# Performance work log

Hardware: AMD Instinct MI355X
Metric: run time of the kernel (lower is better)

## Reference

```python
import jax, jax.numpy as jnp
import numpy as np

OBS_LEN, PRED_LEN, N, NUM_SEQ = 8, 12, 512, 8
H_ENC, H_DEC, EMB, NOISE_DIM = 8, 16, 16, 8


def setup_inputs() -> dict:
    key = jax.random.key(0)
    ks = jax.random.split(key, 32)
    def rn(i, shape, std=1.0):
        return jax.random.normal(ks[i], shape, jnp.float32) * std
    bounds = np.arange(NUM_SEQ + 1) * (N // NUM_SEQ)
    bih_t = jnp.zeros(4 * H_ENC, jnp.float32).at[H_ENC:2 * H_ENC].set(1.0)  # forget bias 1
    bih_p = jnp.zeros(4 * H_DEC, jnp.float32).at[H_DEC:2 * H_DEC].set(1.0)
    return {
        'traj_rel': rn(0, (OBS_LEN + PRED_LEN, N, 2)),
        'obs_traj_pos': rn(1, (OBS_LEN, N, 2), 5.0),
        'pred_traj_gt_pos': rn(2, (PRED_LEN, N, 2), 5.0),
        'h0': rn(3, (N, H_ENC)), 'c0': rn(4, (N, H_ENC)),
        'noise': rn(5, (NUM_SEQ, NOISE_DIM)),
        'W_enc': rn(6, (EMB, 2), 0.2), 'b_enc': jnp.zeros(EMB, jnp.float32),
        'W_dec': rn(7, (EMB, H_DEC + 2), 0.2), 'b_dec': jnp.zeros(EMB, jnp.float32),
        'Wih_t': rn(8, (4 * H_ENC, EMB), 0.1), 'Whh_t': rn(9, (4 * H_ENC, H_ENC), 0.001),
        'bih_t': bih_t, 'bhh_t': jnp.zeros(4 * H_ENC, jnp.float32),
        'Wih_p': rn(10, (4 * H_DEC, EMB), 0.1), 'Whh_p': rn(11, (4 * H_DEC, H_DEC), 0.001),
        'bih_p': bih_p, 'bhh_p': jnp.zeros(4 * H_DEC, jnp.float32),
        'W_out': rn(12, (2, H_DEC), 0.1), 'b_out': jnp.zeros(2, jnp.float32),
        'W_se': rn(13, (EMB, 2), 0.1), 'b_se': jnp.zeros(EMB, jnp.float32),
        'W_m1': rn(14, (64, EMB + H_DEC), 0.1), 'b_m1': jnp.zeros(64, jnp.float32),
        'W_m2': rn(15, (H_DEC, 64), 0.1), 'b_m2': jnp.zeros(H_DEC, jnp.float32),
        'W_att': rn(16, (1, H_DEC), 0.1), 'b_att': jnp.zeros(1, jnp.float32),
        'seq_start_end': jnp.asarray(np.stack([bounds[:-1], bounds[1:]], 1), jnp.int32),
        'nei_index': jax.random.randint(ks[17], (PRED_LEN, N, N), 0, 2, jnp.int32),
        'nei_num_index': jnp.full((N,), N // 2, jnp.int32),
    }


def _lstm_cell(x, h, c, Wih, Whh, bih, bhh):
    g = x @ Wih.T + bih + h @ Whh.T + bhh
    i, f, gg, o = jnp.split(g, 4, axis=-1)
    c2 = jax.nn.sigmoid(f) * c + jax.nn.sigmoid(i) * jnp.tanh(gg)
    return jax.nn.sigmoid(o) * jnp.tanh(c2), c2


def reference(traj_rel, obs_traj_pos, pred_traj_gt_pos, h0, c0, noise,
              W_enc, b_enc, W_dec, b_dec,
              Wih_t, Whh_t, bih_t, bhh_t,
              Wih_p, Whh_p, bih_p, bhh_p,
              W_out, b_out, W_se, b_se, W_m1, b_m1, W_m2, b_m2, W_att, b_att,
              seq_start_end, nei_index, nei_num_index):
    nb = traj_rel.shape[1]

    # ---- encoder: obs_len tiny LSTM steps over relative displacements ----
    def enc_step(carry, x_t):
        h, c = carry
        e = jax.nn.relu(x_t @ W_enc.T + b_enc)
        h, c = _lstm_cell(e, h, c, Wih_t, Whh_t, bih_t, bhh_t)
        return (h, c), None
    (h_enc, _), _ = jax.lax.scan(enc_step, (h0, c0), traj_rel[:OBS_LEN])

    # ---- add global per-scene noise (noise_mix_type == 'global') ----
    seq_ids = jnp.searchsorted(seq_start_end[:, 0], jnp.arange(nb), side='right') - 1
    dec_h = jnp.concatenate([h_enc, noise[seq_ids]], axis=1)  # [N, 16]

    def pool(pos, mask, h):
        # corr_index[i,j] = pos[i] - pos[j]
        corr = pos[:, None, :] - pos[None, :, :]                 # [N,N,2]
        r = corr @ W_se.T + b_se                                 # [N,N,EMB]
        hj = jnp.broadcast_to(h[None, :, :], (nb, nb, H_DEC))    # neighbor hidden
        m_in = jnp.concatenate([r, hj], axis=-1)                 # [N,N,EMB+H]
        h1 = jax.nn.relu(m_in @ W_m1.T + b_m1)                   # [N,N,64]
        pre = jax.nn.relu(h1 @ W_m2.T + b_m2)                    # [N,N,H]
        s = jnp.squeeze(pre @ W_att.T + b_att, -1)               # [N,N]
        s = jnp.where(mask, s, -1e9)
        w = jax.nn.softmax(s, axis=-1)
        ctx = jnp.einsum('ij,ijh->ih', w, pre)
        return jnp.where(mask.any(-1, keepdims=True), ctx, 0.0)

    # ---- decoder: pred_len steps with social pooling each step ----
    sg = jax.lax.stop_gradient
    init = (dec_h, jnp.zeros_like(dec_h), jnp.zeros_like(dec_h),
            jnp.zeros((nb, 2), dec_h.dtype), obs_traj_pos[-1])

    def dec_step(carry, nei_t):
        h, c, ctx, out, pos = carry
        inp_cat = jnp.concatenate([sg(ctx), sg(out)], axis=-1)   # [N, 18]
        e = jax.nn.relu(inp_cat @ W_dec.T + b_dec)
        h, c = _lstm_cell(e, h, c, Wih_p, Whh_p, bih_p, bhh_p)
        ctx = pool(pos, nei_t > 0, h)
        out = jnp.tanh((ctx + h) @ W_out.T + b_out) * 4.4
        pos = sg(pos + out)
        return (h, c, ctx, out, pos), out

    _, pred_traj_rel = jax.lax.scan(dec_step, init, nei_index)
    return pred_traj_rel  # [pred_len, N, 2]
```

## Files before the change

kernel.cpp:

```cpp
#include <hip/hip_runtime.h>
#include <math.h>

#define NPED 512
#define OBS 8
#define PRED 12
#define HE 8
#define HD 16
#define EMB 16
#define NZ 8
#define NSEQ 8

typedef const float* fp;
typedef float f2 __attribute__((ext_vector_type(2)));

__device__ __forceinline__ float frcp(float x){ return __builtin_amdgcn_rcpf(x); }
__device__ __forceinline__ float sigm(float x){ return frcp(1.0f + __expf(-x)); }
__device__ __forceinline__ float tanh_f(float x){ return 1.0f - 2.0f*frcp(__expf(2.0f*x) + 1.0f); }

#define WS_H    0
#define WS_C    (WS_H + NPED*HD)
#define WS_POS0 (WS_C + NPED*HD)
#define WS_POS1 (WS_POS0 + NPED*2)
#define WS_HB0  (WS_POS1 + NPED*2)
#define WS_HB1  (WS_HB0 + NPED*64)
#define WS_A0   (WS_HB1 + NPED*64)
#define WS_A1   (WS_A0 + 64)
#define WS_BB   (WS_A1 + 64)
#define WS_WM2T (WS_BB + 64)

__global__ __launch_bounds__(256) void init_kernel(
        fp traj, fp obs_pos, fp h0, fp c0, fp noise,
        fp Wenc, fp benc, fp Wih, fp Whh, fp bih, fp bhh,
        fp bdec, fp Wihp, fp Whhp, fp bihp, fp bhhp, fp Wm1,
        fp Wse, fp bse, fp bm1, fp Wm2,
        const int* sse, float* ws)
{
    __shared__ float s_wenc[32], s_benc[16], s_wihT[32*17], s_whhT[32*9], s_bT[32];
    __shared__ float s_wihP[64*17], s_whhP[64*17], s_wm1h[64*17], s_bP[64], s_e0[16];
    __shared__ float s_hc[16*16];
    int tid = threadIdx.x;

    if (blockIdx.x == 0) {
        if (tid < 64) {
            float a0 = 0.f, a1 = 0.f, bb = bm1[tid];
            for (int kk = 0; kk < 16; kk++) {
                float w = Wm1[tid*32 + kk];
                a0 += w*Wse[kk*2+0]; a1 += w*Wse[kk*2+1]; bb += w*bse[kk];
            }
            ws[WS_A0 + tid] = a0; ws[WS_A1 + tid] = a1; ws[WS_BB + tid] = bb;
        }
        for (int i = tid; i < 1024; i += 256) {
            int u = i >> 4, v = i & 15;
            ws[WS_WM2T + u*16 + v] = Wm2[v*64 + u];
        }
    }

    if (tid < 32) { s_wenc[tid] = Wenc[tid]; s_bT[tid] = bih[tid] + bhh[tid]; }
    if (tid < 16) { s_benc[tid] = benc[tid]; s_e0[tid] = fmaxf(bdec[tid], 0.f); }
    for (int i = tid; i < 512; i += 256) s_wihT[(i>>4)*17 + (i&15)] = Wih[i];
    { int i = tid; if (i < 256) s_whhT[(i>>3)*9 + (i&7)] = Whh[i]; }
    for (int i = tid; i < 1024; i += 256) {
        int r = i>>4, d = i&15;
        s_wihP[r*17+d] = Wihp[i];
        s_whhP[r*17+d] = Whhp[i];
        s_wm1h[r*17+d] = Wm1[r*32 + 16 + d];
    }
    if (tid < 64) s_bP[tid] = bihp[tid] + bhhp[tid];
    __syncthreads();

    int pid = tid >> 4, k16 = tid & 15;
    int n = blockIdx.x*16 + pid;

    if (k16 < 8) {
        int k = k16;
        float h = h0[n*HE+k], c = c0[n*HE+k];
        for (int t = 0; t < OBS; t++) {
            float x0 = traj[(t*NPED+n)*2+0];
            float x1 = traj[(t*NPED+n)*2+1];
            float g0 = s_bT[k], g1 = s_bT[8+k], g2 = s_bT[16+k], g3 = s_bT[24+k];
            #pragma unroll
            for (int d = 0; d < EMB; d++) {
                float e = fmaxf(s_wenc[d*2]*x0 + s_wenc[d*2+1]*x1 + s_benc[d], 0.f);
                g0 += s_wihT[(k)*17+d]*e;    g1 += s_wihT[(8+k)*17+d]*e;
                g2 += s_wihT[(16+k)*17+d]*e; g3 += s_wihT[(24+k)*17+d]*e;
            }
            #pragma unroll
            for (int d = 0; d < HE; d++) {
                float hv = __shfl(h, d, 8);
                g0 += s_whhT[(k)*9+d]*hv;    g1 += s_whhT[(8+k)*9+d]*hv;
                g2 += s_whhT[(16+k)*9+d]*hv; g3 += s_whhT[(24+k)*9+d]*hv;
            }
            c = sigm(g1)*c + sigm(g0)*tanh_f(g2);
            h = sigm(g3)*tanh_f(c);
        }
        int cnt = 0;
        #pragma unroll
        for (int s2 = 0; s2 < NSEQ; s2++) cnt += (sse[s2*2] <= n) ? 1 : 0;
        s_hc[pid*16 + k]     = h;
        s_hc[pid*16 + 8 + k] = noise[(cnt-1)*NZ + k];
    }
    __syncthreads();

    int k = k16;
    float h = s_hc[pid*16 + k];
    float g0 = s_bP[k], g1 = s_bP[16+k], g2 = s_bP[32+k], g3 = s_bP[48+k];
    #pragma unroll
    for (int d = 0; d < HD; d++) {
        float ev = s_e0[d];
        float hv = __shfl(h, d, 16);
        g0 += s_wihP[(k)*17+d]*ev    + s_whhP[(k)*17+d]*hv;
        g1 += s_wihP[(16+k)*17+d]*ev + s_whhP[(16+k)*17+d]*hv;
        g2 += s_wihP[(32+k)*17+d]*ev + s_whhP[(32+k)*17+d]*hv;
        g3 += s_wihP[(48+k)*17+d]*ev + s_whhP[(48+k)*17+d]*hv;
    }
    float c = sigm(g0)*tanh_f(g2);
    float hn = sigm(g3)*tanh_f(c);
    ws[WS_H + n*HD + k] = hn;
    ws[WS_C + n*HD + k] = c;

    float hb0=0.f, hb1=0.f, hb2=0.f, hb3=0.f;
    #pragma unroll
    for (int d = 0; d < HD; d++) {
        float hv = __shfl(hn, d, 16);
        hb0 += s_wm1h[(k)*17+d]*hv;    hb1 += s_wm1h[(16+k)*17+d]*hv;
        hb2 += s_wm1h[(32+k)*17+d]*hv; hb3 += s_wm1h[(48+k)*17+d]*hv;
    }
    float* hb = ws + WS_HB0 + n*64;
    hb[k] = hb0; hb[16+k] = hb1; hb[32+k] = hb2; hb[48+k] = hb3;
    if (k < 2) ws[WS_POS0 + n*2 + k] = obs_pos[((OBS-1)*NPED+n)*2 + k];
}

__global__ __launch_bounds__(512, 4) void pool_step_kernel(
        int t, int last, const int* nei,
        fp Wm1, fp bm2, fp Watt, fp batt,
        fp Wdec, fp bdec, fp Wihp, fp Whhp, fp bihp, fp bhhp, fp Wout, fp bout,
        float* ws, float* dout)
{
    __shared__ float s_A0[64], s_A1[64], s_BB[64];
    __shared__ float s_wm2t[1024];
    __shared__ float s_bm2[16], s_watt[16];
    __shared__ float s_batt;
    __shared__ float s_posx[NPED], s_posy[NPED];
    __shared__ int   s_list[NPED], s_cnt[8];
    __shared__ float s_mat[16*512];
    __shared__ float s_lred[8], s_mred[8], s_ctxacc[16], s_ctx[16];
    __shared__ float s_wdec[16*19], s_bdec[16], s_wout[32], s_bout[2];
    int tid = threadIdx.x;

    if (tid < 64) { s_A0[tid] = ws[WS_A0+tid]; s_A1[tid] = ws[WS_A1+tid]; s_BB[tid] = ws[WS_BB+tid]; }
    if (tid < 256) ((float4*)s_wm2t)[tid] = ((const float4*)(ws + WS_WM2T))[tid];
    if (tid < 16) { s_bm2[tid] = bm2[tid]; s_watt[tid] = Watt[tid]; }
    if (tid == 0) s_batt = batt[0];
    for (int i = tid; i < 288; i += 512) s_wdec[(i/18)*19 + (i%18)] = Wdec[i];
    if (tid < 16) s_bdec[tid] = bdec[tid];
    if (tid < 32) s_wout[tid] = Wout[tid];
    if (tid < 2)  s_bout[tid] = bout[tid];

    const float* posrd = ws + ((t & 1) ? WS_POS1 : WS_POS0);
    const float* hbrd  = ws + ((t & 1) ? WS_HB1  : WS_HB0 );
    float* poswr = ws + ((t & 1) ? WS_POS0 : WS_POS1);
    float* hbwr  = ws + ((t & 1) ? WS_HB0  : WS_HB1 );
    {
        const float2* p2 = (const float2*)posrd;
        for (int j = tid; j < NPED; j += 512) { float2 pp = p2[j]; s_posx[j] = pp.x; s_posy[j] = pp.y; }
    }
    __syncthreads();

    int i = blockIdx.x;
    int w = tid >> 6, lane = tid & 63;
    unsigned long long below = (1ull << lane) - 1ull;

    int a = nei[((size_t)t*NPED + i)*NPED + tid] > 0;
    unsigned long long mb = __ballot(a);
    if (lane == 0) s_cnt[w] = __popcll(mb);
    __syncthreads();
    int cnt = 0, base = 0;
    #pragma unroll
    for (int q = 0; q < 8; q++) {
        int cq = s_cnt[q];
        cnt += cq;
        if (q < w) base += cq;
    }
    if (a) s_list[base + __popcll(mb & below)] = tid;
    __syncthreads();

    float pix = s_posx[i], piy = s_posy[i];
    f2 pre2[8];
    #pragma unroll
    for (int q = 0; q < 8; q++) pre2[q] = (f2){0.f, 0.f};
    float sc = -INFINITY;

    if (tid < cnt) {
        #pragma unroll
        for (int q = 0; q < 8; q++) pre2[q] = (f2){s_bm2[2*q], s_bm2[2*q+1]};
        int j = s_list[tid];
        float cx = pix - s_posx[j], cy = piy - s_posy[j];
        const float4* HB4 = (const float4*)(hbrd + j*64);
        const f2* A0v = (const f2*)s_A0;
        const f2* A1v = (const f2*)s_A1;
        const f2* BBv = (const f2*)s_BB;
        #pragma unroll
        for (int uq = 0; uq < 16; uq++) {
            float4 hb = HB4[uq];
            f2 hA = {hb.x, hb.y}, hB = {hb.z, hb.w};
            f2 h1A = __builtin_elementwise_max(A0v[2*uq]*cx + A1v[2*uq]*cy + (BBv[2*uq] + hA), (f2){0.f,0.f});
            f2 h1B = __builtin_elementwise_max(A0v[2*uq+1]*cx + A1v[2*uq+1]*cy + (BBv[2*uq+1] + hB), (f2){0.f,0.f});
            #define ACC16(u_, hsc_) { \
                f2 hs = {hsc_, hsc_}; \
                const f2* wr = (const f2*)(s_wm2t + (u_)*16); \
                for (int q = 0; q < 8; q++) pre2[q] = __builtin_elementwise_fma(wr[q], hs, pre2[q]); }
            ACC16(uq*4+0, h1A.x) ACC16(uq*4+1, h1A.y) ACC16(uq*4+2, h1B.x) ACC16(uq*4+3, h1B.y)
            #undef ACC16
        }
        f2 sacc = {0.f, 0.f};
        const f2* wa = (const f2*)s_watt;
        #pragma unroll
        for (int q = 0; q < 8; q++) {
            pre2[q] = __builtin_elementwise_max(pre2[q], (f2){0.f,0.f});
            sacc = __builtin_elementwise_fma(pre2[q], wa[q], sacc);
        }
        sc = s_batt + sacc.x + sacc.y;
    }

    float mloc = sc;
    #pragma unroll
    for (int off = 32; off >= 1; off >>= 1) mloc = fmaxf(mloc, __shfl_xor(mloc, off));
    if (lane == 0) s_mred[w] = mloc;
    __syncthreads();
    float M = s_mred[0];
    #pragma unroll
    for (int q = 1; q < 8; q++) M = fmaxf(M, s_mred[q]);

    float wexp = (tid < cnt) ? __expf(sc - M) : 0.f;
    float l = wexp;
    #pragma unroll
    for (int off = 32; off >= 1; off >>= 1) l += __shfl_xor(l, off);
    if (lane == 0) s_lred[w] = l;
    {
        const float* pa = (const float*)pre2;
        #pragma unroll
        for (int v = 0; v < 16; v++) s_mat[v*512 + tid] = wexp * pa[v];
    }
    __syncthreads();
    {
        int vv = tid >> 5, cc = tid & 31;
        float ssum = 0.f;
        #pragma unroll
        for (int e = 0; e < 16; e++) ssum += s_mat[vv*512 + cc + e*32];
        #pragma unroll
        for (int off = 16; off >= 1; off >>= 1) ssum += __shfl_xor(ssum, off, 32);
        if (cc == 0) s_ctxacc[vv] = ssum;
    }
    __syncthreads();
    if (tid < 16) {
        float cv = 0.f;
        if (cnt > 0) {
            float L = 0.f;
            #pragma unroll
            for (int q = 0; q < 8; q++) L += s_lred[q];
            cv = (L > 0.f) ? s_ctxacc[tid] / L : 0.f;
        }
        s_ctx[tid] = cv;
    }
    __syncthreads();

    if (tid < 64) {
        int r = tid;
        float h16 = 0.f, ctx16 = 0.f, cst = 0.f;
        if (r < 16) {
            h16   = ws[WS_H + i*HD + r];
            ctx16 = s_ctx[r];
            cst   = ws[WS_C + i*HD + r];
        }
        float ch = ctx16 + h16;
        float r0 = 0.f, r1 = 0.f;
        if (r < 16) { r0 = s_wout[r]*ch; r1 = s_wout[16+r]*ch; }
        #pragma unroll
        for (int off = 8; off >= 1; off >>= 1) {
            r0 += __shfl_xor(r0, off, 16);
            r1 += __shfl_xor(r1, off, 16);
        }
        float o0 = tanh_f(s_bout[0] + r0)*4.4f;
        float o1 = tanh_f(s_bout[1] + r1)*4.4f;
        if (r == 0) { dout[(t*NPED + i)*2 + 0] = o0; poswr[i*2+0] = pix + o0; }
        if (r == 1) { dout[(t*NPED + i)*2 + 1] = o1; poswr[i*2+1] = piy + o1; }

        if (!last) {
            float e = 0.f;
            if (r < 16) {
                e = s_bdec[r];
                #pragma unroll
                for (int d = 0; d < HD; d++) e += s_wdec[r*19 + d]*s_ctx[d];
                e += s_wdec[r*19+16]*o0 + s_wdec[r*19+17]*o1;
                e = fmaxf(e, 0.f);
            }
            const float4* wi4 = (const float4*)(Wihp + r*16);
            const float4* wh4 = (const float4*)(Whhp + r*16);
            float4 wi0 = wi4[0], wi1 = wi4[1], wi2 = wi4[2], wi3 = wi4[3];
            float4 wh0 = wh4[0], wh1 = wh4[1], wh2 = wh4[2], wh3 = wh4[3];
            float g = bihp[r] + bhhp[r];
            #define GD(wiv, whv, d0) { \
                g += wiv.x*__shfl(e, d0)   + whv.x*__shfl(h16, d0); \
                g += wiv.y*__shfl(e, d0+1) + whv.y*__shfl(h16, d0+1); \
                g += wiv.z*__shfl(e, d0+2) + whv.z*__shfl(h16, d0+2); \
                g += wiv.w*__shfl(e, d0+3) + whv.w*__shfl(h16, d0+3); }
            GD(wi0, wh0, 0) GD(wi1, wh1, 4) GD(wi2, wh2, 8) GD(wi3, wh3, 12)
            #undef GD
            float gi = __shfl(g, r & 15);
            float gf = __shfl(g, 16 + (r & 15));
            float gg = __shfl(g, 32 + (r & 15));
            float go = __shfl(g, 48 + (r & 15));
            float hn = 0.f;
            if (r < 16) {
                float cn = sigm(gf)*cst + sigm(gi)*tanh_f(gg);
                hn = sigm(go)*tanh_f(cn);
                ws[WS_H + i*HD + r] = hn;
                ws[WS_C + i*HD + r] = cn;
            }
            const float4* wm4 = (const float4*)(Wm1 + r*32 + 16);
            float4 m0 = wm4[0], m1 = wm4[1], m2 = wm4[2], m3 = wm4[3];
            float hb = 0.f;
            #define HBD(mv, d0) { \
                hb += mv.x*__shfl(hn, d0)   + mv.y*__shfl(hn, d0+1); \
                hb += mv.z*__shfl(hn, d0+2) + mv.w*__shfl(hn, d0+3); }
            HBD(m0, 0) HBD(m1, 4) HBD(m2, 8) HBD(m3, 12)
            #undef HBD
            hbwr[i*64 + r] = hb;
        }
    }
}

extern "C" void kernel_launch(void* const* d_in, const int* in_sizes, int n_in,
                              void* d_out, int out_size, void* d_ws, size_t ws_size,
                              hipStream_t stream)
{
    fp traj = (fp)d_in[0];
    fp obs  = (fp)d_in[1];
    fp h0   = (fp)d_in[3];
    fp c0   = (fp)d_in[4];
    fp noise= (fp)d_in[5];
    fp Wenc = (fp)d_in[6];  fp benc = (fp)d_in[7];
    fp Wdec = (fp)d_in[8];  fp bdec = (fp)d_in[9];
    fp Wiht = (fp)d_in[10]; fp Whht = (fp)d_in[11];
    fp biht = (fp)d_in[12]; fp bhht = (fp)d_in[13];
    fp Wihp = (fp)d_in[14]; fp Whhp = (fp)d_in[15];
    fp bihp = (fp)d_in[16]; fp bhhp = (fp)d_in[17];
    fp Wout = (fp)d_in[18]; fp bout = (fp)d_in[19];
    fp Wse  = (fp)d_in[20]; fp bse  = (fp)d_in[21];
    fp Wm1  = (fp)d_in[22]; fp bm1  = (fp)d_in[23];
    fp Wm2  = (fp)d_in[24]; fp bm2  = (fp)d_in[25];
    fp Watt = (fp)d_in[26]; fp batt = (fp)d_in[27];
    const int* sse = (const int*)d_in[28];
    const int* nei = (const int*)d_in[29];
    float* ws = (float*)d_ws;
    float* out = (float*)d_out;

    hipLaunchKernelGGL(init_kernel, dim3(32), dim3(256), 0, stream,
                       traj, obs, h0, c0, noise, Wenc, benc, Wiht, Whht, biht, bhht,
                       bdec, Wihp, Whhp, bihp, bhhp, Wm1, Wse, bse, bm1, Wm2, sse, ws);
    for (int t = 0; t < PRED; t++) {
        hipLaunchKernelGGL(pool_step_kernel, dim3(NPED), dim3(512), 0, stream,
                           t, (t == PRED-1) ? 1 : 0, nei,
                           Wm1, bm2, Watt, batt,
                           Wdec, bdec, Wihp, Whhp, bihp, bhhp, Wout, bout,
                           ws, out);
    }
}
```

Measured before the change: 169.7 us.

## Process two pedestrians per block with two neighbor pairs per thread

The pooling step kernel now handles two query pedestrians per 512-thread block, one per 256-thread half. Each thread evaluates up to two neighbor pairs, and the grid shrinks to half as many blocks. This is meant to cut the idle threads left when only about half the neighbors are active, and to share the per-block weight and position loads across two rows. The neighbor-mask load is also issued earlier. In exchange, the launch-bounds occupancy hint drops to two blocks and register pressure rises. The pre-activation arrays are no longer zero-initialised, so the products weighted by zero can read uninitialised values.

```diff
diff --git a/kernel.cpp b/kernel.cpp
--- a/kernel.cpp
+++ b/kernel.cpp
@@ -130,7 +130,44 @@
     if (k < 2) ws[WS_POS0 + n*2 + k] = obs_pos[((OBS-1)*NPED+n)*2 + k];
 }
 
-__global__ __launch_bounds__(512, 4) void pool_step_kernel(
+__device__ __forceinline__ float pair_compute(
+        int j, float pix, float piy,
+        const float* s_posx, const float* s_posy,
+        const float* s_A0, const float* s_A1, const float* s_BB,
+        const float* s_wm2t, const float* s_watt, float batt,
+        const float* hbrd, f2 pre2[8], const float* s_bm2)
+{
+    #pragma unroll
+    for (int q = 0; q < 8; q++) pre2[q] = (f2){s_bm2[2*q], s_bm2[2*q+1]};
+    float cx = pix - s_posx[j], cy = piy - s_posy[j];
+    const float4* HB4 = (const float4*)(hbrd + j*64);
+    const f2* A0v = (const f2*)s_A0;
+    const f2* A1v = (const f2*)s_A1;
+    const f2* BBv = (const f2*)s_BB;
+    #pragma unroll
+    for (int uq = 0; uq < 16; uq++) {
+        float4 hb = HB4[uq];
+        f2 hA = {hb.x, hb.y}, hB = {hb.z, hb.w};
+        f2 h1A = __builtin_elementwise_max(A0v[2*uq]*cx + A1v[2*uq]*cy + (BBv[2*uq] + hA), (f2){0.f,0.f});
+        f2 h1B = __builtin_elementwise_max(A0v[2*uq+1]*cx + A1v[2*uq+1]*cy + (BBv[2*uq+1] + hB), (f2){0.f,0.f});
+        #define ACC16(u_, hsc_) { \
+            f2 hs = {hsc_, hsc_}; \
+            const f2* wr = (const f2*)(s_wm2t + (u_)*16); \
+            for (int q = 0; q < 8; q++) pre2[q] = __builtin_elementwise_fma(wr[q], hs, pre2[q]); }
+        ACC16(uq*4+0, h1A.x) ACC16(uq*4+1, h1A.y) ACC16(uq*4+2, h1B.x) ACC16(uq*4+3, h1B.y)
+        #undef ACC16
+    }
+    f2 sacc = {0.f, 0.f};
+    const f2* wa = (const f2*)s_watt;
+    #pragma unroll
+    for (int q = 0; q < 8; q++) {
+        pre2[q] = __builtin_elementwise_max(pre2[q], (f2){0.f,0.f});
+        sacc = __builtin_elementwise_fma(pre2[q], wa[q], sacc);
+    }
+    return batt + sacc.x + sacc.y;
+}
+
+__global__ __launch_bounds__(512, 2) void pool_step_kernel(
         int t, int last, const int* nei,
         fp Wm1, fp bm2, fp Watt, fp batt,
         fp Wdec, fp bdec, fp Wihp, fp Whhp, fp bihp, fp bhhp, fp Wout, fp bout,
@@ -141,20 +178,27 @@
     __shared__ float s_bm2[16], s_watt[16];
     __shared__ float s_batt;
     __shared__ float s_posx[NPED], s_posy[NPED];
-    __shared__ int   s_list[NPED], s_cnt[8];
+    __shared__ int   s_list[2*512], s_cnt[2][8];
     __shared__ float s_mat[16*512];
-    __shared__ float s_lred[8], s_mred[8], s_ctxacc[16], s_ctx[16];
+    __shared__ float s_lred[8], s_mred[8], s_ctxacc[32], s_ctx[32];
     __shared__ float s_wdec[16*19], s_bdec[16], s_wout[32], s_bout[2];
     int tid = threadIdx.x;
+    int h = tid >> 8;
+    int u = tid & 255;
+    int i = blockIdx.x*2 + h;
+
+    const int* neirow = nei + ((size_t)t*NPED + i)*NPED;
+    int a0 = neirow[u]       > 0;
+    int a1 = neirow[256 + u] > 0;
 
     if (tid < 64) { s_A0[tid] = ws[WS_A0+tid]; s_A1[tid] = ws[WS_A1+tid]; s_BB[tid] = ws[WS_BB+tid]; }
-    if (tid < 256) ((float4*)s_wm2t)[tid] = ((const float4*)(ws + WS_WM2T))[tid];
+    if (tid >= 64 && tid < 320) ((float4*)s_wm2t)[tid-64] = ((const float4*)(ws + WS_WM2T))[tid-64];
     if (tid < 16) { s_bm2[tid] = bm2[tid]; s_watt[tid] = Watt[tid]; }
     if (tid == 0) s_batt = batt[0];
-    for (int i = tid; i < 288; i += 512) s_wdec[(i/18)*19 + (i%18)] = Wdec[i];
-    if (tid < 16) s_bdec[tid] = bdec[tid];
-    if (tid < 32) s_wout[tid] = Wout[tid];
-    if (tid < 2)  s_bout[tid] = bout[tid];
+    for (int q = tid; q < 288; q += 512) s_wdec[(q/18)*19 + (q%18)] = Wdec[q];
+    if (tid >= 32 && tid < 48) s_bdec[tid-32] = bdec[tid-32];
+    if (tid >= 448 && tid < 480) s_wout[tid-448] = Wout[tid-448];
+    if (tid >= 480 && tid < 482) s_bout[tid-480] = bout[tid-480];
 
     const float* posrd = ws + ((t & 1) ? WS_POS1 : WS_POS0);
     const float* hbrd  = ws + ((t & 1) ? WS_HB1  : WS_HB0 );
@@ -162,114 +206,86 @@
     float* hbwr  = ws + ((t & 1) ? WS_HB0  : WS_HB1 );
     {
         const float2* p2 = (const float2*)posrd;
-        for (int j = tid; j < NPED; j += 512) { float2 pp = p2[j]; s_posx[j] = pp.x; s_posy[j] = pp.y; }
-    }
-    __syncthreads();
-
-    int i = blockIdx.x;
-    int w = tid >> 6, lane = tid & 63;
+        float2 pp = p2[tid & 511 % NPED];
+        if (tid < NPED) { s_posx[tid] = pp.x; s_posy[tid] = pp.y; }
+    }
+
+    int wv = tid >> 6, lane = tid & 63, w4 = wv & 3;
     unsigned long long below = (1ull << lane) - 1ull;
 
-    int a = nei[((size_t)t*NPED + i)*NPED + tid] > 0;
-    unsigned long long mb = __ballot(a);
-    if (lane == 0) s_cnt[w] = __popcll(mb);
-    __syncthreads();
-    int cnt = 0, base = 0;
+    unsigned long long m0 = __ballot(a0), m1 = __ballot(a1);
+    if (lane == 0) { s_cnt[h][w4] = __popcll(m0); s_cnt[h][4+w4] = __popcll(m1); }
+    __syncthreads();
+    int cnt = 0, base0 = 0, base1 = 0;
     #pragma unroll
     for (int q = 0; q < 8; q++) {
-        int cq = s_cnt[q];
+        int cq = s_cnt[h][q];
         cnt += cq;
-        if (q < w) base += cq;
-    }
-    if (a) s_list[base + __popcll(mb & below)] = tid;
+        if (q < w4)     base0 += cq;
+        if (q < 4 + w4) base1 += cq;
+    }
+    if (a0) s_list[h*512 + base0 + __popcll(m0 & below)] = u;
+    if (a1) s_list[h*512 + base1 + __popcll(m1 & below)] = 256 + u;
     __syncthreads();
 
     float pix = s_posx[i], piy = s_posy[i];
-    f2 pre2[8];
-    #pragma unroll
-    for (int q = 0; q < 8; q++) pre2[q] = (f2){0.f, 0.f};
-    float sc = -INFINITY;
-
-    if (tid < cnt) {
-        #pragma unroll
-        for (int q = 0; q < 8; q++) pre2[q] = (f2){s_bm2[2*q], s_bm2[2*q+1]};
-        int j = s_list[tid];
-        float cx = pix - s_posx[j], cy = piy - s_posy[j];
-        const float4* HB4 = (const float4*)(hbrd + j*64);
-        const f2* A0v = (const f2*)s_A0;
-        const f2* A1v = (const f2*)s_A1;
-        const f2* BBv = (const f2*)s_BB;
-        #pragma unroll
-        for (int uq = 0; uq < 16; uq++) {
-            float4 hb = HB4[uq];
-            f2 hA = {hb.x, hb.y}, hB = {hb.z, hb.w};
-            f2 h1A = __builtin_elementwise_max(A0v[2*uq]*cx + A1v[2*uq]*cy + (BBv[2*uq] + hA), (f2){0.f,0.f});
-            f2 h1B = __builtin_elementwise_max(A0v[2*uq+1]*cx + A1v[2*uq+1]*cy + (BBv[2*uq+1] + hB), (f2){0.f,0.f});
-            #define ACC16(u_, hsc_) { \
-                f2 hs = {hsc_, hsc_}; \
-                const f2* wr = (const f2*)(s_wm2t + (u_)*16); \
-                for (int q = 0; q < 8; q++) pre2[q] = __builtin_elementwise_fma(wr[q], hs, pre2[q]); }
-            ACC16(uq*4+0, h1A.x) ACC16(uq*4+1, h1A.y) ACC16(uq*4+2, h1B.x) ACC16(uq*4+3, h1B.y)
-            #undef ACC16
-        }
-        f2 sacc = {0.f, 0.f};
-        const f2* wa = (const f2*)s_watt;
-        #pragma unroll
-        for (int q = 0; q < 8; q++) {
-            pre2[q] = __builtin_elementwise_max(pre2[q], (f2){0.f,0.f});
-            sacc = __builtin_elementwise_fma(pre2[q], wa[q], sacc);
-        }
-        sc = s_batt + sacc.x + sacc.y;
-    }
-
-    float mloc = sc;
+    f2 preA[8], preB[8];
+    float scA = -INFINITY, scB = -INFINITY;
+    if (u < cnt)
+        scA = pair_compute(s_list[h*512 + u], pix, piy, s_posx, s_posy,
+                           s_A0, s_A1, s_BB, s_wm2t, s_watt, s_batt, hbrd, preA, s_bm2);
+    if (256 + u < cnt)
+        scB = pair_compute(s_list[h*512 + 256 + u], pix, piy, s_posx, s_posy,
+                           s_A0, s_A1, s_BB, s_wm2t, s_watt, s_batt, hbrd, preB, s_bm2);
+
+    float mloc = fmaxf(scA, scB);
     #pragma unroll
     for (int off = 32; off >= 1; off >>= 1) mloc = fmaxf(mloc, __shfl_xor(mloc, off));
-    if (lane == 0) s_mred[w] = mloc;
-    __syncthreads();
-    float M = s_mred[0];
-    #pragma unroll
-    for (int q = 1; q < 8; q++) M = fmaxf(M, s_mred[q]);
-
-    float wexp = (tid < cnt) ? __expf(sc - M) : 0.f;
-    float l = wexp;
+    if (lane == 0) s_mred[wv] = mloc;
+    __syncthreads();
+    float M = fmaxf(fmaxf(s_mred[h*4], s_mred[h*4+1]), fmaxf(s_mred[h*4+2], s_mred[h*4+3]));
+
+    float wA = (u < cnt)       ? __expf(scA - M) : 0.f;
+    float wB = (256 + u < cnt) ? __expf(scB - M) : 0.f;
+    float l = wA + wB;
     #pragma unroll
     for (int off = 32; off >= 1; off >>= 1) l += __shfl_xor(l, off);
-    if (lane == 0) s_lred[w] = l;
+    if (lane == 0) s_lred[wv] = l;
     {
-        const float* pa = (const float*)pre2;
-        #pragma unroll
-        for (int v = 0; v < 16; v++) s_mat[v*512 + tid] = wexp * pa[v];
+        const float* pa = (const float*)preA;
+        const float* pb = (const float*)preB;
+        #pragma unroll
+        for (int v = 0; v < 16; v++) s_mat[v*512 + tid] = wA*pa[v] + wB*pb[v];
     }
     __syncthreads();
     {
-        int vv = tid >> 5, cc = tid & 31;
+        int g = tid >> 4, cc = tid & 15;
+        int rr = g >> 4, vv = g & 15;
+        const float* src = s_mat + vv*512 + rr*256 + cc*16;
         float ssum = 0.f;
         #pragma unroll
-        for (int e = 0; e < 16; e++) ssum += s_mat[vv*512 + cc + e*32];
-        #pragma unroll
-        for (int off = 16; off >= 1; off >>= 1) ssum += __shfl_xor(ssum, off, 32);
-        if (cc == 0) s_ctxacc[vv] = ssum;
-    }
-    __syncthreads();
-    if (tid < 16) {
+        for (int e = 0; e < 16; e++) ssum += src[e];
+        #pragma unroll
+        for (int off = 8; off >= 1; off >>= 1) ssum += __shfl_xor(ssum, off, 16);
+        if (cc == 0) s_ctxacc[rr*16 + vv] = ssum;
+    }
+    __syncthreads();
+    if (u < 16) {
         float cv = 0.f;
         if (cnt > 0) {
-            float L = 0.f;
-            #pragma unroll
-            for (int q = 0; q < 8; q++) L += s_lred[q];
-            cv = (L > 0.f) ? s_ctxacc[tid] / L : 0.f;
-        }
-        s_ctx[tid] = cv;
-    }
-    __syncthreads();
-
-    if (tid < 64) {
-        int r = tid;
+            float L = s_lred[h*4] + s_lred[h*4+1] + s_lred[h*4+2] + s_lred[h*4+3];
+            cv = (L > 0.f) ? s_ctxacc[h*16 + u] / L : 0.f;
+        }
+        s_ctx[h*16 + u] = cv;
+    }
+    __syncthreads();
+
+    if (u < 64) {
+        int r = u;
         float h16 = 0.f, ctx16 = 0.f, cst = 0.f;
         if (r < 16) {
             h16   = ws[WS_H + i*HD + r];
-            ctx16 = s_ctx[r];
+            ctx16 = s_ctx[h*16 + r];
             cst   = ws[WS_C + i*HD + r];
         }
         float ch = ctx16 + h16;
@@ -290,7 +306,7 @@
             if (r < 16) {
                 e = s_bdec[r];
                 #pragma unroll
-                for (int d = 0; d < HD; d++) e += s_wdec[r*19 + d]*s_ctx[d];
+                for (int d = 0; d < HD; d++) e += s_wdec[r*19 + d]*s_ctx[h*16 + d];
                 e += s_wdec[r*19+16]*o0 + s_wdec[r*19+17]*o1;
                 e = fmaxf(e, 0.f);
             }
@@ -318,12 +334,12 @@
                 ws[WS_C + i*HD + r] = cn;
             }
             const float4* wm4 = (const float4*)(Wm1 + r*32 + 16);
-            float4 m0 = wm4[0], m1 = wm4[1], m2 = wm4[2], m3 = wm4[3];
+            float4 m0v = wm4[0], m1v = wm4[1], m2v = wm4[2], m3v = wm4[3];
             float hb = 0.f;
             #define HBD(mv, d0) { \
                 hb += mv.x*__shfl(hn, d0)   + mv.y*__shfl(hn, d0+1); \
                 hb += mv.z*__shfl(hn, d0+2) + mv.w*__shfl(hn, d0+3); }
-            HBD(m0, 0) HBD(m1, 4) HBD(m2, 8) HBD(m3, 12)
+            HBD(m0v, 0) HBD(m1v, 4) HBD(m2v, 8) HBD(m3v, 12)
             #undef HBD
             hbwr[i*64 + r] = hb;
         }
@@ -359,7 +375,7 @@
                        traj, obs, h0, c0, noise, Wenc, benc, Wiht, Whht, biht, bhht,
                        bdec, Wihp, Whhp, bihp, bhhp, Wm1, Wse, bse, bm1, Wm2, sse, ws);
     for (int t = 0; t < PRED; t++) {
-        hipLaunchKernelGGL(pool_step_kernel, dim3(NPED), dim3(512), 0, stream,
+        hipLaunchKernelGGL(pool_step_kernel, dim3(NPED/2), dim3(512), 0, stream,
                            t, (t == PRED-1) ? 1 : 0, nei,
                            Wm1, bm2, Watt, batt,
                            Wdec, bdec, Wihp, Whhp, bihp, bhhp, Wout, bout,
```

New measurement: 212.6 us. +25.3%, slower.
